# Kernel optimization log

Measured on AMD Instinct MI355X. Metric: run time of the kernel, lower is better.

Reference implementation:

```python
import jax, jax.numpy as jnp
import numpy as np

D_K = 64
SCALE = D_K ** (-0.5)
B, H, S = 2, 16, 2048


def setup_inputs() -> dict:
    key = jax.random.key(0)
    kq, kk, kv = jax.random.split(key, 3)
    q = jax.random.normal(kq, (B, H, S, D_K), dtype=jnp.float32)
    k = jax.random.normal(kk, (B, H, S, D_K), dtype=jnp.float32)
    v = jax.random.normal(kv, (B, H, S, D_K), dtype=jnp.float32)
    # causal mask: True means masked (matches torch masked_fill semantics)
    mask = jnp.triu(jnp.ones((S, S), dtype=bool), k=1)[None, None]  # [1,1,S,S]
    return {"q": q, "k": k, "v": v, "mask": mask}


def reference(q, k, v, mask) -> jnp.ndarray:
    # scores = q @ k^T  -> [B,H,S,S]
    scores = jnp.einsum("bhqd,bhkd->bhqk", q, k)
    # masked_fill(mask, -inf), then scale (as written in the source),
    # then softmax over the key axis. -inf * scale stays -inf.
    scores = jnp.where(mask, -jnp.inf, scores)
    attn = jax.nn.softmax(SCALE * scores, axis=-1)
    return jnp.einsum("bhqk,bhkd->bhqd", attn, v)
```

## Files before the change

kernel.cpp:

```cpp
#include <hip/hip_runtime.h>
#include <hip/hip_bf16.h>
#include <math.h>


constexpr int S  = 2048;
constexpr int D  = 64;
constexpr int BH = 32;
constexpr float SCALE = 0.125f;
constexpr float LOG2E = 1.4426950408889634f;
constexpr float QPRE  = SCALE * LOG2E;
constexpr int PSTR = 72;

typedef __attribute__((ext_vector_type(8))) short bf16x8;
typedef __attribute__((ext_vector_type(4))) short bf16x4;
typedef __attribute__((ext_vector_type(4))) float f32x4;

#if __has_builtin(__builtin_amdgcn_exp2f)
#define EXP2F(x) __builtin_amdgcn_exp2f(x)
#else
#define EXP2F(x) exp2f(x)
#endif

__device__ __forceinline__ short f2bf(float x) {
    union { __hip_bfloat16 b; short s; } u; u.b = __float2bfloat16(x); return u.s;
}

__device__ __forceinline__ void gload_lds16(const void* g, void* lds) {
    __builtin_amdgcn_global_load_lds(
        (const __attribute__((address_space(1))) unsigned int*)g,
        (__attribute__((address_space(3))) unsigned int*)lds, 16, 0, 0);
}

__global__ __launch_bounds__(256) void preconv_25993142075924(
    const float* __restrict__ Kg, const float* __restrict__ Vg,
    short* __restrict__ Kb, short* __restrict__ VT)
{
    const int kt = blockIdx.x, bh = blockIdx.y, tid = threadIdx.x;
    __shared__ float lt[64 * 65];
    const float* kp = Kg + (size_t)bh * S * D;
    const float* vp = Vg + (size_t)bh * S * D;
    short* kb = Kb + (size_t)bh * S * D;
    short* vt = VT + (size_t)bh * D * S;
    #pragma unroll
    for (int e = 0; e < 4; ++e) {
        int idx = (tid + e * 256) * 4;
        int r = idx >> 6, c = idx & 63;
        f32x4 k4 = *(const f32x4*)(kp + (size_t)(kt * 64 + r) * D + c);
        bf16x4 kb4;
        kb4[0] = f2bf(k4[0]); kb4[1] = f2bf(k4[1]);
        kb4[2] = f2bf(k4[2]); kb4[3] = f2bf(k4[3]);
        *(bf16x4*)(kb + (size_t)(kt * 64 + r) * D + c) = kb4;
        f32x4 v4 = *(const f32x4*)(vp + (size_t)(kt * 64 + r) * D + c);
        lt[(c + 0) * 65 + r] = v4[0];
        lt[(c + 1) * 65 + r] = v4[1];
        lt[(c + 2) * 65 + r] = v4[2];
        lt[(c + 3) * 65 + r] = v4[3];
    }
    __syncthreads();
    #pragma unroll
    for (int e = 0; e < 2; ++e) {
        int tt = tid + e * 256;
        int d  = tt >> 3;
        int j0 = (tt & 7) * 8;
        bf16x8 o;
        #pragma unroll
        for (int jj = 0; jj < 8; ++jj)
            o[jj] = f2bf(lt[d * 65 + j0 + jj]);
        *(bf16x8*)(vt + (size_t)d * S + kt * 64 + j0) = o;
    }
}

__global__ __launch_bounds__(256, 3) void attn_fwd_v5_25993142075924(
    const float* __restrict__ Qg, const short* __restrict__ Kb,
    const short* __restrict__ VT, float* __restrict__ Og)
{
    const int bh  = blockIdx.x;
    const int pa  = blockIdx.y;
    const int tid = threadIdx.x;
    const int wv  = tid >> 6;
    const int ln  = tid & 63;
    const int c16 = ln & 15;
    const int qd  = ln >> 4;

    __shared__ __align__(16) short lk[2][64 * 64];
    __shared__ __align__(16) short lv[2][64 * 64];
    __shared__ __align__(16) short lp[4 * 16 * PSTR];
    short* lpw = lp + wv * 16 * PSTR;

    const float* qp = Qg + (size_t)bh * S * D;
    const short* kp = Kb + (size_t)bh * S * D;
    const short* vp = VT + (size_t)bh * D * S;
    float*       op = Og + (size_t)bh * S * D;

    const int qbs[2] = { pa, 31 - pa };

    const int srow0 = wv * 16 + (ln >> 3);
    const int sgrp0 = (ln & 7) ^ (srow0 & 7);
    const int srow1 = srow0 + 8;
    const int sgrp1 = (ln & 7) ^ (srow1 & 7);

    for (int ph = 0; ph < 2; ++ph) {
        const int qb  = qbs[ph];
        const int nkt = qb + 1;
        const int q0  = (qb * 4 + wv) * 16;

        bf16x8 qf[2];
        {
            const float* src = qp + (size_t)(q0 + c16) * D + qd * 8;
            #pragma unroll
            for (int khf = 0; khf < 2; ++khf) {
                f32x4 a = *(const f32x4*)(src + khf * 32);
                f32x4 b = *(const f32x4*)(src + khf * 32 + 4);
                bf16x8 f;
                f[0] = f2bf(a[0] * QPRE); f[1] = f2bf(a[1] * QPRE);
                f[2] = f2bf(a[2] * QPRE); f[3] = f2bf(a[3] * QPRE);
                f[4] = f2bf(b[0] * QPRE); f[5] = f2bf(b[1] * QPRE);
                f[6] = f2bf(b[2] * QPRE); f[7] = f2bf(b[3] * QPRE);
                qf[khf] = f;
            }
        }

        f32x4 oacc[4] = {{0,0,0,0},{0,0,0,0},{0,0,0,0},{0,0,0,0}};
        float lpart[4] = {0.f, 0.f, 0.f, 0.f};

        {
            const size_t kbase = (size_t)0 * 64;
            gload_lds16(kp + (size_t)(srow0)*D + sgrp0 * 8, &lk[0][(wv * 16 + 0) * 64]);
            gload_lds16(vp + (size_t)srow0 * S + kbase + sgrp0 * 8, &lv[0][(wv * 16 + 0) * 64]);
            gload_lds16(kp + (size_t)(srow1)*D + sgrp1 * 8, &lk[0][(wv * 16 + 8) * 64]);
            gload_lds16(vp + (size_t)srow1 * S + kbase + sgrp1 * 8, &lv[0][(wv * 16 + 8) * 64]);
        }
        __syncthreads();

        for (int kt = 0; kt < nkt; ++kt) {
            const int cur = kt & 1;
            if (kt + 1 < nkt) {
                const int nxt = cur ^ 1;
                const size_t kb0 = (size_t)(kt + 1) * 64;
                gload_lds16(kp + (kb0 + srow0) * D + sgrp0 * 8, &lk[nxt][(wv * 16 + 0) * 64]);
                gload_lds16(vp + (size_t)srow0 * S + kb0 + sgrp0 * 8, &lv[nxt][(wv * 16 + 0) * 64]);
                gload_lds16(kp + (kb0 + srow1) * D + sgrp1 * 8, &lk[nxt][(wv * 16 + 8) * 64]);
                gload_lds16(vp + (size_t)srow1 * S + kb0 + sgrp1 * 8, &lv[nxt][(wv * 16 + 8) * 64]);
            }

            float t[4][4];
            #pragma unroll
            for (int nt = 0; nt < 4; ++nt) {
                const int row = nt * 16 + c16;
                f32x4 acc = {0,0,0,0};
                #pragma unroll
                for (int khf = 0; khf < 2; ++khf) {
                    const int g = (khf * 4 + qd) ^ (row & 7);
                    bf16x8 kf = *(const bf16x8*)&lk[cur][row * 64 + g * 8];
                    acc = __builtin_amdgcn_mfma_f32_16x16x32_bf16(qf[khf], kf, acc, 0, 0, 0);
                }
                t[nt][0] = acc[0]; t[nt][1] = acc[1]; t[nt][2] = acc[2]; t[nt][3] = acc[3];
            }

            if (kt == qb) {
                #pragma unroll
                for (int nt = 0; nt < 4; ++nt) {
                    int j = kt * 64 + nt * 16 + c16;
                    #pragma unroll
                    for (int r = 0; r < 4; ++r)
                        if (j > q0 + qd * 4 + r) t[nt][r] = -INFINITY;
                }
            }

            float pval[4][4];
            #pragma unroll
            for (int nt = 0; nt < 4; ++nt)
                #pragma unroll
                for (int r = 0; r < 4; ++r) {
                    float p = EXP2F(t[nt][r]);
                    pval[nt][r] = p;
                    lpart[r] += p;
                }

            #pragma unroll
            for (int nt = 0; nt < 4; ++nt)
                #pragma unroll
                for (int r = 0; r < 4; ++r)
                    lpw[(qd * 4 + r) * PSTR + nt * 16 + c16] = f2bf(pval[nt][r]);
            bf16x8 pf[2];
            #pragma unroll
            for (int khf = 0; khf < 2; ++khf)
                pf[khf] = *(const bf16x8*)&lpw[c16 * PSTR + khf * 32 + qd * 8];

            #pragma unroll
            for (int dt = 0; dt < 4; ++dt) {
                const int row = dt * 16 + c16;
                #pragma unroll
                for (int khf = 0; khf < 2; ++khf) {
                    const int g = (khf * 4 + qd) ^ (row & 7);
                    bf16x8 vf = *(const bf16x8*)&lv[cur][row * 64 + g * 8];
                    oacc[dt] = __builtin_amdgcn_mfma_f32_16x16x32_bf16(pf[khf], vf, oacc[dt], 0, 0, 0);
                }
            }

            __syncthreads();
        }

        #pragma unroll
        for (int r = 0; r < 4; ++r) {
            float s = lpart[r];
            s += __shfl_xor(s, 1);
            s += __shfl_xor(s, 2);
            s += __shfl_xor(s, 4);
            s += __shfl_xor(s, 8);
            float inv = 1.0f / s;
            float* dst = op + (size_t)(q0 + qd * 4 + r) * D;
            #pragma unroll
            for (int dt = 0; dt < 4; ++dt)
                dst[dt * 16 + c16] = oacc[dt][r] * inv;
        }
    }
}

__global__ __launch_bounds__(256) void attn_fwd_v1_25993142075924(
    const float* __restrict__ Qg, const float* __restrict__ Kg,
    const float* __restrict__ Vg, float* __restrict__ Og)
{
    constexpr int KSTR = 72;
    constexpr int BQ = 64, BK = 64;
    const int qt  = blockIdx.x;
    const int bh  = blockIdx.y;
    const int tid = threadIdx.x;
    const int wv  = tid >> 6;
    const int ln  = tid & 63;
    const int c16 = ln & 15;
    const int qd  = ln >> 4;

    __shared__ __align__(16) __hip_bfloat16 lk [BK][KSTR];
    __shared__ __align__(16) __hip_bfloat16 lvt[D ][KSTR];
    __shared__ __align__(16) __hip_bfloat16 lp [4][16][KSTR];

    const size_t hoff = (size_t)bh * S * D;
    const float* qp = Qg + hoff;
    const float* kp = Kg + hoff;
    const float* vp = Vg + hoff;
    float*       op = Og + hoff;
    const int q0 = qt * BQ;

    bf16x8 qf[2];
    {
        const float* src = qp + (size_t)(q0 + wv*16 + c16) * D + qd*8;
        #pragma unroll
        for (int kh = 0; kh < 2; ++kh) {
            f32x4 a = *(const f32x4*)(src + kh*32);
            f32x4 b = *(const f32x4*)(src + kh*32 + 4);
            bf16x8 f;
            f[0]=f2bf(a[0]*QPRE); f[1]=f2bf(a[1]*QPRE); f[2]=f2bf(a[2]*QPRE); f[3]=f2bf(a[3]*QPRE);
            f[4]=f2bf(b[0]*QPRE); f[5]=f2bf(b[1]*QPRE); f[6]=f2bf(b[2]*QPRE); f[7]=f2bf(b[3]*QPRE);
            qf[kh] = f;
        }
    }

    f32x4 oacc[4] = {{0,0,0,0},{0,0,0,0},{0,0,0,0},{0,0,0,0}};
    float mrun[4] = {-INFINITY,-INFINITY,-INFINITY,-INFINITY};
    float lrun[4] = {0.f,0.f,0.f,0.f};

    const int nkt = qt + 1;
    for (int kt = 0; kt < nkt; ++kt) {
        __syncthreads();
        #pragma unroll
        for (int e = 0; e < 4; ++e) {
            int idx = (tid + e*256) * 4;
            int row = idx >> 6, col = idx & 63;
            f32x4 k4 = *(const f32x4*)(kp + (size_t)(kt*BK + row)*D + col);
            bf16x4 kb;
            kb[0]=f2bf(k4[0]); kb[1]=f2bf(k4[1]); kb[2]=f2bf(k4[2]); kb[3]=f2bf(k4[3]);
            *(bf16x4*)&lk[row][col] = kb;
            f32x4 v4 = *(const f32x4*)(vp + (size_t)(kt*BK + row)*D + col);
            lvt[col+0][row] = __float2bfloat16(v4[0]);
            lvt[col+1][row] = __float2bfloat16(v4[1]);
            lvt[col+2][row] = __float2bfloat16(v4[2]);
            lvt[col+3][row] = __float2bfloat16(v4[3]);
        }
        __syncthreads();

        float t[4][4];
        #pragma unroll
        for (int nt = 0; nt < 4; ++nt) {
            f32x4 acc = {0,0,0,0};
            #pragma unroll
            for (int kh = 0; kh < 2; ++kh) {
                bf16x8 kf = *(const bf16x8*)&lk[nt*16 + c16][kh*32 + qd*8];
                acc = __builtin_amdgcn_mfma_f32_16x16x32_bf16(qf[kh], kf, acc, 0, 0, 0);
            }
            #pragma unroll
            for (int r = 0; r < 4; ++r) t[nt][r] = acc[r];
        }
        if (kt == nkt - 1) {
            #pragma unroll
            for (int nt = 0; nt < 4; ++nt) {
                int j = kt*BK + nt*16 + c16;
                #pragma unroll
                for (int r = 0; r < 4; ++r)
                    if (j > q0 + wv*16 + qd*4 + r) t[nt][r] = -INFINITY;
            }
        }

        float pval[4][4];
        #pragma unroll
        for (int r = 0; r < 4; ++r) {
            float tm = fmaxf(fmaxf(t[0][r], t[1][r]), fmaxf(t[2][r], t[3][r]));
            tm = fmaxf(tm, __shfl_xor(tm, 1));
            tm = fmaxf(tm, __shfl_xor(tm, 2));
            tm = fmaxf(tm, __shfl_xor(tm, 4));
            tm = fmaxf(tm, __shfl_xor(tm, 8));
            float mnew  = fmaxf(mrun[r], tm);
            float alpha = exp2f(mrun[r] - mnew);
            mrun[r] = mnew;
            float rs = 0.f;
            #pragma unroll
            for (int nt = 0; nt < 4; ++nt) {
                float p = exp2f(t[nt][r] - mnew);
                pval[nt][r] = p;
                rs += p;
            }
            rs += __shfl_xor(rs, 1);
            rs += __shfl_xor(rs, 2);
            rs += __shfl_xor(rs, 4);
            rs += __shfl_xor(rs, 8);
            lrun[r] = lrun[r] * alpha + rs;
            #pragma unroll
            for (int dt = 0; dt < 4; ++dt) oacc[dt][r] *= alpha;
        }

        #pragma unroll
        for (int nt = 0; nt < 4; ++nt)
            #pragma unroll
            for (int r = 0; r < 4; ++r)
                lp[wv][qd*4 + r][nt*16 + c16] = __float2bfloat16(pval[nt][r]);
        bf16x8 pf[2];
        #pragma unroll
        for (int kh = 0; kh < 2; ++kh)
            pf[kh] = *(const bf16x8*)&lp[wv][c16][kh*32 + qd*8];

        #pragma unroll
        for (int dt = 0; dt < 4; ++dt) {
            #pragma unroll
            for (int kh = 0; kh < 2; ++kh) {
                bf16x8 vf = *(const bf16x8*)&lvt[dt*16 + c16][kh*32 + qd*8];
                oacc[dt] = __builtin_amdgcn_mfma_f32_16x16x32_bf16(pf[kh], vf, oacc[dt], 0, 0, 0);
            }
        }
    }

    #pragma unroll
    for (int r = 0; r < 4; ++r) {
        float inv = 1.0f / lrun[r];
        float* dst = op + (size_t)(q0 + wv*16 + qd*4 + r) * D;
        #pragma unroll
        for (int dt = 0; dt < 4; ++dt)
            dst[dt*16 + c16] = oacc[dt][r] * inv;
    }
}

extern "C" void kernel_launch(void* const* d_in, const int* in_sizes, int n_in,
                              void* d_out, int out_size, void* d_ws, size_t ws_size,
                              hipStream_t stream) {
    const float* q = (const float*)d_in[0];
    const float* k = (const float*)d_in[1];
    const float* v = (const float*)d_in[2];
    float* out = (float*)d_out;
    const size_t elems = (size_t)BH * S * D;
    const size_t need  = 2 * elems * sizeof(short);
    if (ws_size >= need) {
        short* Kb = (short*)d_ws;
        short* VT = Kb + elems;
        preconv_25993142075924<<<dim3(S / 64, BH), 256, 0, stream>>>(k, v, Kb, VT);
        attn_fwd_v5_25993142075924<<<dim3(BH, 16), 256, 0, stream>>>(q, Kb, VT, out);
    } else {
        attn_fwd_v1_25993142075924<<<dim3(S / 64, BH), 256, 0, stream>>>(q, k, v, out);
    }
}
```

Before: 138.5 us.

## Process two adjacent query blocks per 512-thread workgroup sharing K/V tiles

```diff
diff --git a/kernel.cpp b/kernel.cpp
--- a/kernel.cpp
+++ b/kernel.cpp
@@ -70,21 +70,27 @@
     }
 }
 
-__global__ __launch_bounds__(256, 3) void attn_fwd_v5_25993142075924(
+__global__ __launch_bounds__(512, 4) void attn_fwd_v6_25993142075924(
     const float* __restrict__ Qg, const short* __restrict__ Kb,
     const short* __restrict__ VT, float* __restrict__ Og)
 {
     const int bh  = blockIdx.x;
-    const int pa  = blockIdx.y;
+    const int p   = 15 - (int)blockIdx.y;
     const int tid = threadIdx.x;
     const int wv  = tid >> 6;
+    const int strip = wv & 3;
+    const int qhalf = wv >> 2;
     const int ln  = tid & 63;
     const int c16 = ln & 15;
     const int qd  = ln >> 4;
 
+    const int qb  = 2 * p + qhalf;
+    const int q0  = qb * 64 + strip * 16;
+    const int nkt = 2 * p + 2;
+
     __shared__ __align__(16) short lk[2][64 * 64];
     __shared__ __align__(16) short lv[2][64 * 64];
-    __shared__ __align__(16) short lp[4 * 16 * PSTR];
+    __shared__ __align__(16) short lp[8 * 16 * PSTR];
     short* lpw = lp + wv * 16 * PSTR;
 
     const float* qp = Qg + (size_t)bh * S * D;
@@ -92,57 +98,42 @@
     const short* vp = VT + (size_t)bh * D * S;
     float*       op = Og + (size_t)bh * S * D;
 
-    const int qbs[2] = { pa, 31 - pa };
-
-    const int srow0 = wv * 16 + (ln >> 3);
-    const int sgrp0 = (ln & 7) ^ (srow0 & 7);
-    const int srow1 = srow0 + 8;
-    const int sgrp1 = (ln & 7) ^ (srow1 & 7);
-
-    for (int ph = 0; ph < 2; ++ph) {
-        const int qb  = qbs[ph];
-        const int nkt = qb + 1;
-        const int q0  = (qb * 4 + wv) * 16;
-
-        bf16x8 qf[2];
-        {
-            const float* src = qp + (size_t)(q0 + c16) * D + qd * 8;
-            #pragma unroll
-            for (int khf = 0; khf < 2; ++khf) {
-                f32x4 a = *(const f32x4*)(src + khf * 32);
-                f32x4 b = *(const f32x4*)(src + khf * 32 + 4);
-                bf16x8 f;
-                f[0] = f2bf(a[0] * QPRE); f[1] = f2bf(a[1] * QPRE);
-                f[2] = f2bf(a[2] * QPRE); f[3] = f2bf(a[3] * QPRE);
-                f[4] = f2bf(b[0] * QPRE); f[5] = f2bf(b[1] * QPRE);
-                f[6] = f2bf(b[2] * QPRE); f[7] = f2bf(b[3] * QPRE);
-                qf[khf] = f;
-            }
-        }
-
-        f32x4 oacc[4] = {{0,0,0,0},{0,0,0,0},{0,0,0,0},{0,0,0,0}};
-        float lpart[4] = {0.f, 0.f, 0.f, 0.f};
-
-        {
-            const size_t kbase = (size_t)0 * 64;
-            gload_lds16(kp + (size_t)(srow0)*D + sgrp0 * 8, &lk[0][(wv * 16 + 0) * 64]);
-            gload_lds16(vp + (size_t)srow0 * S + kbase + sgrp0 * 8, &lv[0][(wv * 16 + 0) * 64]);
-            gload_lds16(kp + (size_t)(srow1)*D + sgrp1 * 8, &lk[0][(wv * 16 + 8) * 64]);
-            gload_lds16(vp + (size_t)srow1 * S + kbase + sgrp1 * 8, &lv[0][(wv * 16 + 8) * 64]);
-        }
-        __syncthreads();
-
-        for (int kt = 0; kt < nkt; ++kt) {
-            const int cur = kt & 1;
-            if (kt + 1 < nkt) {
-                const int nxt = cur ^ 1;
-                const size_t kb0 = (size_t)(kt + 1) * 64;
-                gload_lds16(kp + (kb0 + srow0) * D + sgrp0 * 8, &lk[nxt][(wv * 16 + 0) * 64]);
-                gload_lds16(vp + (size_t)srow0 * S + kb0 + sgrp0 * 8, &lv[nxt][(wv * 16 + 0) * 64]);
-                gload_lds16(kp + (kb0 + srow1) * D + sgrp1 * 8, &lk[nxt][(wv * 16 + 8) * 64]);
-                gload_lds16(vp + (size_t)srow1 * S + kb0 + sgrp1 * 8, &lv[nxt][(wv * 16 + 8) * 64]);
-            }
-
+    const int srow = wv * 8 + (ln >> 3);
+    const int sgrp = (ln & 7) ^ (srow & 7);
+
+    bf16x8 qf[2];
+    {
+        const float* src = qp + (size_t)(q0 + c16) * D + qd * 8;
+        #pragma unroll
+        for (int khf = 0; khf < 2; ++khf) {
+            f32x4 a = *(const f32x4*)(src + khf * 32);
+            f32x4 b = *(const f32x4*)(src + khf * 32 + 4);
+            bf16x8 f;
+            f[0] = f2bf(a[0] * QPRE); f[1] = f2bf(a[1] * QPRE);
+            f[2] = f2bf(a[2] * QPRE); f[3] = f2bf(a[3] * QPRE);
+            f[4] = f2bf(b[0] * QPRE); f[5] = f2bf(b[1] * QPRE);
+            f[6] = f2bf(b[2] * QPRE); f[7] = f2bf(b[3] * QPRE);
+            qf[khf] = f;
+        }
+    }
+
+    f32x4 oacc[4] = {{0,0,0,0},{0,0,0,0},{0,0,0,0},{0,0,0,0}};
+    float lpart[4] = {0.f, 0.f, 0.f, 0.f};
+
+    gload_lds16(kp + (size_t)srow * D + sgrp * 8, &lk[0][(wv * 8) * 64]);
+    gload_lds16(vp + (size_t)srow * S + sgrp * 8, &lv[0][(wv * 8) * 64]);
+    __syncthreads();
+
+    for (int kt = 0; kt < nkt; ++kt) {
+        const int cur = kt & 1;
+        if (kt + 1 < nkt) {
+            const int nxt = cur ^ 1;
+            const size_t kb0 = (size_t)(kt + 1) * 64;
+            gload_lds16(kp + (kb0 + srow) * D + sgrp * 8, &lk[nxt][(wv * 8) * 64]);
+            gload_lds16(vp + (size_t)srow * S + kb0 + sgrp * 8, &lv[nxt][(wv * 8) * 64]);
+        }
+
+        if (kt <= qb) {
             float t[4][4];
             #pragma unroll
             for (int nt = 0; nt < 4; ++nt) {
@@ -172,9 +163,9 @@
             for (int nt = 0; nt < 4; ++nt)
                 #pragma unroll
                 for (int r = 0; r < 4; ++r) {
-                    float p = EXP2F(t[nt][r]);
-                    pval[nt][r] = p;
-                    lpart[r] += p;
+                    float pv = EXP2F(t[nt][r]);
+                    pval[nt][r] = pv;
+                    lpart[r] += pv;
                 }
 
             #pragma unroll
@@ -197,23 +188,23 @@
                     oacc[dt] = __builtin_amdgcn_mfma_f32_16x16x32_bf16(pf[khf], vf, oacc[dt], 0, 0, 0);
                 }
             }
-
-            __syncthreads();
-        }
-
-        #pragma unroll
-        for (int r = 0; r < 4; ++r) {
-            float s = lpart[r];
-            s += __shfl_xor(s, 1);
-            s += __shfl_xor(s, 2);
-            s += __shfl_xor(s, 4);
-            s += __shfl_xor(s, 8);
-            float inv = 1.0f / s;
-            float* dst = op + (size_t)(q0 + qd * 4 + r) * D;
-            #pragma unroll
-            for (int dt = 0; dt < 4; ++dt)
-                dst[dt * 16 + c16] = oacc[dt][r] * inv;
-        }
+        }
+
+        __syncthreads();
+    }
+
+    #pragma unroll
+    for (int r = 0; r < 4; ++r) {
+        float s = lpart[r];
+        s += __shfl_xor(s, 1);
+        s += __shfl_xor(s, 2);
+        s += __shfl_xor(s, 4);
+        s += __shfl_xor(s, 8);
+        float inv = 1.0f / s;
+        float* dst = op + (size_t)(q0 + qd * 4 + r) * D;
+        #pragma unroll
+        for (int dt = 0; dt < 4; ++dt)
+            dst[dt * 16 + c16] = oacc[dt][r] * inv;
     }
 }
 
@@ -315,9 +306,9 @@
             float rs = 0.f;
             #pragma unroll
             for (int nt = 0; nt < 4; ++nt) {
-                float p = exp2f(t[nt][r] - mnew);
-                pval[nt][r] = p;
-                rs += p;
+                float pv = exp2f(t[nt][r] - mnew);
+                pval[nt][r] = pv;
+                rs += pv;
             }
             rs += __shfl_xor(rs, 1);
             rs += __shfl_xor(rs, 2);
@@ -371,7 +362,7 @@
         short* Kb = (short*)d_ws;
         short* VT = Kb + elems;
         preconv_25993142075924<<<dim3(S / 64, BH), 256, 0, stream>>>(k, v, Kb, VT);
-        attn_fwd_v5_25993142075924<<<dim3(BH, 16), 256, 0, stream>>>(q, Kb, VT, out);
+        attn_fwd_v6_25993142075924<<<dim3(BH, 16), 512, 0, stream>>>(q, Kb, VT, out);
     } else {
         attn_fwd_v1_25993142075924<<<dim3(S / 64, BH), 256, 0, stream>>>(q, k, v, out);
     }
```

Measured after the change: 140.9 us. Within noise of the previous version (+1.7%).
